# Kernel optimization log

Measured on AMD Instinct MI355X. Metric: run time of the kernel, lower is better.

The kernel has to match this reference:

```python
import jax, jax.numpy as jnp
import numpy as np


def _gcn_conv(X, src, dst, norm, W, n_nodes):
    # gather + normalized aggregate (SpMM) then dense linear (GEMM)
    msg = X[src] * norm[:, None]                       # [E, F]
    agg = jax.ops.segment_sum(msg, dst, num_segments=n_nodes)  # [N, F]
    return agg @ W                                     # [N, F_out]


def setup_inputs() -> dict:
    key = jax.random.key(0)
    k1, k2, k3, k4, k5 = jax.random.split(key, 5)
    N, E, D_IN, D_HID, D_OUT = 50000, 800000, 128, 128, 64
    X = jax.random.normal(k1, (N, D_IN), dtype=jnp.float32)
    edge_index = jax.random.randint(k2, (2, E), 0, N, dtype=jnp.int64)
    s = 1.0 / np.sqrt(D_IN)
    W1 = jax.random.normal(k3, (D_IN, D_HID), dtype=jnp.float32) * s
    W2 = jax.random.normal(k4, (D_HID, D_HID), dtype=jnp.float32) * s
    W3 = jax.random.normal(k5, (D_HID, D_OUT), dtype=jnp.float32) * s
    return {"X": X, "edge_index": edge_index, "W1": W1, "W2": W2, "W3": W3}


def reference(X, edge_index, W1, W2, W3):
    n_nodes = X.shape[0]
    src, dst = edge_index[0], edge_index[1]
    # symmetric degree normalization D^-1/2 A D^-1/2 (degrees from edge list)
    ones = jnp.ones(src.shape[0], dtype=X.dtype)
    deg = jax.ops.segment_sum(ones, dst, num_segments=n_nodes)
    deg = jnp.maximum(deg, 1.0)
    dinv = jax.lax.rsqrt(deg)
    norm = dinv[src] * dinv[dst]                       # [E]
    h = jax.nn.relu(_gcn_conv(X, src, dst, norm, W1, n_nodes))
    h = jax.nn.relu(_gcn_conv(h, src, dst, norm, W2, n_nodes))
    h = jax.nn.relu(_gcn_conv(h, src, dst, norm, W3, n_nodes))
    return jax.nn.softmax(h, axis=-1)
```

## Files before the change

### kernel.cpp

```cpp
#include <hip/hip_runtime.h>
#include <hip/hip_bf16.h>

typedef __attribute__((ext_vector_type(8))) short short8;
typedef __attribute__((ext_vector_type(4))) short short4v;
typedef __attribute__((ext_vector_type(4))) float f32x4;

static inline size_t ws_align(size_t x) { return (x + 511) & ~((size_t)511); }

static __device__ inline unsigned short f2bf(float f) {
    __hip_bfloat16 h = __float2bfloat16(f);
    return __builtin_bit_cast(unsigned short, h);
}
static __device__ inline float bfbits2f(unsigned short u) {
    unsigned x = ((unsigned)u) << 16;
    return __builtin_bit_cast(float, x);
}

static __device__ inline int sniff_fp32(const unsigned short* __restrict__ w1) {
    int i = threadIdx.x & 63;
    unsigned e = (w1[2 * i] >> 7) & 0xFF;
    unsigned long long m = __ballot(e >= 100 && e <= 130);
    return (__popcll(m) < 48) ? 1 : 0;
}
static __device__ inline int sniff_is64(const unsigned int* __restrict__ ei) {
    int i = threadIdx.x & 63;
    unsigned long long m = __ballot(ei[2 * i + 1] == 0u);
    return (__popcll(m) >= 48) ? 1 : 0;
}

__global__ void hist_kernel(const int* __restrict__ ei,
                            int* __restrict__ counts, int* __restrict__ loff, int E) {
    int is64 = sniff_is64((const unsigned int*)ei);
    int e = blockIdx.x * blockDim.x + threadIdx.x;
    if (e < E) {
        int d = is64 ? ei[2 * (size_t)E + 2 * e] : ei[(size_t)E + e];
        loff[e] = atomicAdd(&counts[d], 1);
    }
}

__global__ __launch_bounds__(256) void alloc_kernel(const int* __restrict__ counts,
                                                    float* __restrict__ dinv,
                                                    int2* __restrict__ rc,
                                                    int* __restrict__ total, int N) {
    int n = blockIdx.x * blockDim.x + threadIdx.x;
    int lane = threadIdx.x & 63;
    int c = (n < N) ? counts[n] : 0;
    if (n < N) {
        int d = (c < 1) ? 1 : c;
        dinv[n] = rsqrtf((float)d);
    }
    int incl = c;
#pragma unroll
    for (int off = 1; off < 64; off <<= 1) {
        int v = __shfl_up(incl, off, 64);
        if (lane >= off) incl += v;
    }
    int wavetot = __shfl(incl, 63, 64);
    int base = 0;
    if (lane == 0) base = atomicAdd(total, wavetot);
    base = __shfl(base, 0, 64);
    if (n < N) rc[n] = make_int2(base + incl - c, c);
}

__global__ void fill_kernel(const int* __restrict__ ei,
                            const float* __restrict__ dinv, const int2* __restrict__ rc,
                            const int* __restrict__ loff, int2* __restrict__ edgedat, int E) {
    int is64 = sniff_is64((const unsigned int*)ei);
    int e = blockIdx.x * blockDim.x + threadIdx.x;
    if (e < E) {
        int s, d;
        if (is64) {
            s = ei[2 * e];
            d = ei[2 * (size_t)E + 2 * e];
        } else {
            s = ei[e];
            d = ei[(size_t)E + e];
        }
        int pos = rc[d].x + loff[e];
        float wt = dinv[s] * dinv[d];
        edgedat[pos] = make_int2(s, __float_as_int(wt));
    }
}


template <int FOUT>
__global__ __launch_bounds__(256) void gemm_kernel(const void* __restrict__ Araw, int a_follows,
                                                   const void* __restrict__ Wraw,
                                                   const unsigned short* __restrict__ w1sniff,
                                                   unsigned short* __restrict__ out, int Nrows) {
    constexpr int K = 128;
    constexpr int NT = FOUT / 16;
    constexpr int LDB = K + 8;
    __shared__ __align__(16) unsigned short bt[FOUT * LDB];

    const int tid = threadIdx.x;
    const int in_fp32 = sniff_fp32(w1sniff);
    const int a_fp32 = a_follows & in_fp32;

    constexpr int TOT4 = K * FOUT / 4;
    if (in_fp32) {
        const float* Wf = (const float*)Wraw;
        for (int i = tid; i < TOT4; i += 256) {
            int idx = i * 4;
            int k = idx / FOUT;
            int n = idx & (FOUT - 1);
            float4 v = *(const float4*)(const void*)(Wf + idx);
            bt[(n + 0) * LDB + k] = f2bf(v.x);
            bt[(n + 1) * LDB + k] = f2bf(v.y);
            bt[(n + 2) * LDB + k] = f2bf(v.z);
            bt[(n + 3) * LDB + k] = f2bf(v.w);
        }
    } else {
        const unsigned short* Ws = (const unsigned short*)Wraw;
        for (int i = tid; i < TOT4; i += 256) {
            int idx = i * 4;
            int k = idx / FOUT;
            int n = idx & (FOUT - 1);
            short4v v = *(const short4v*)(const void*)(Ws + idx);
#pragma unroll
            for (int j = 0; j < 4; j++) bt[(n + j) * LDB + k] = ((const unsigned short*)&v)[j];
        }
    }

    const int wave = tid >> 6;
    const int lane = tid & 63;
    const int quad = lane >> 4;
    const int r16 = lane & 15;

    short8 afrag[2][4];
#pragma unroll
    for (int t = 0; t < 2; t++) {
        int arow = blockIdx.x * 128 + t * 64 + wave * 16 + r16;
        if (arow > Nrows - 1) arow = Nrows - 1;
        if (a_fp32) {
            const float* Ap = (const float*)Araw + (size_t)arow * K + quad * 8;
#pragma unroll
            for (int kk = 0; kk < 4; kk++) {
                float4 f0 = *(const float4*)(const void*)(Ap + kk * 32);
                float4 f1 = *(const float4*)(const void*)(Ap + kk * 32 + 4);
                short8 r;
                r[0] = (short)f2bf(f0.x); r[1] = (short)f2bf(f0.y);
                r[2] = (short)f2bf(f0.z); r[3] = (short)f2bf(f0.w);
                r[4] = (short)f2bf(f1.x); r[5] = (short)f2bf(f1.y);
                r[6] = (short)f2bf(f1.z); r[7] = (short)f2bf(f1.w);
                afrag[t][kk] = r;
            }
        } else {
            const unsigned short* Ap = (const unsigned short*)Araw + (size_t)arow * K + quad * 8;
#pragma unroll
            for (int kk = 0; kk < 4; kk++) afrag[t][kk] = *(const short8*)(const void*)(Ap + kk * 32);
        }
    }

    __syncthreads();

    f32x4 acc[2][NT];
#pragma unroll
    for (int t = 0; t < 2; t++)
#pragma unroll
        for (int nt = 0; nt < NT; nt++) acc[t][nt] = (f32x4){0.f, 0.f, 0.f, 0.f};

#pragma unroll
    for (int kk = 0; kk < 4; kk++) {
#pragma unroll
        for (int nt = 0; nt < NT; nt++) {
            short8 b = *(const short8*)(const void*)(&bt[(nt * 16 + r16) * LDB + kk * 32 + quad * 8]);
#pragma unroll
            for (int t = 0; t < 2; t++)
                acc[t][nt] = __builtin_amdgcn_mfma_f32_16x16x32_bf16(afrag[t][kk], b, acc[t][nt], 0, 0, 0);
        }
    }

#pragma unroll
    for (int t = 0; t < 2; t++) {
#pragma unroll
        for (int nt = 0; nt < NT; nt++) {
#pragma unroll
            for (int r = 0; r < 4; r++) {
                float v = acc[t][nt][r];
                float o = __shfl_xor(v, 1, 64);
                int row = blockIdx.x * 128 + t * 64 + wave * 16 + quad * 4 + r;
                if (((lane & 1) == 0) && row < Nrows) {
                    __hip_bfloat162 pk;
                    pk.x = __float2bfloat16(v);
                    pk.y = __float2bfloat16(o);
                    *(__hip_bfloat162*)(out + (size_t)row * FOUT + nt * 16 + r16) = pk;
                }
            }
        }
    }
}


__global__ __launch_bounds__(256) void spmm128_kernel(const int2* __restrict__ edgedat,
                                                      const int2* __restrict__ rc,
                                                      const unsigned short* __restrict__ Hin,
                                                      unsigned short* __restrict__ Hout, int N) {
    int wid = (blockIdx.x * 256 + threadIdx.x) >> 6;
    int lane = threadIdx.x & 63;
    int half = lane >> 5;
    int li = lane & 31;
    int n = wid * 2 + half;
    int nc = (n < N) ? n : (N - 1);
    int2 r_ = rc[nc];
    int start = r_.x;
    int len = (n < N) ? r_.y : 0;
    int maxlen = max(len, __shfl_xor(len, 32, 64));

    float a0 = 0.f, a1 = 0.f, a2 = 0.f, a3 = 0.f;
    for (int j = 0; j < maxlen; j += 8) {
        int2 ed[8];
#pragma unroll
        for (int u = 0; u < 8; u++) {
            int jj = j + u;
            int idx = (jj < len) ? (start + jj) : start;
            ed[u] = edgedat[idx];
        }
        short4v hv[8];
#pragma unroll
        for (int u = 0; u < 8; u++) {
            int s = ed[u].x;
            s = (s < 0) ? 0 : ((s > N - 1) ? (N - 1) : s);
            hv[u] = *(const short4v*)(const void*)(Hin + (size_t)s * 128 + li * 4);
        }
#pragma unroll
        for (int u = 0; u < 8; u++) {
            float w = ((j + u) < len) ? __int_as_float(ed[u].y) : 0.f;
            a0 += w * bfbits2f((unsigned short)hv[u][0]);
            a1 += w * bfbits2f((unsigned short)hv[u][1]);
            a2 += w * bfbits2f((unsigned short)hv[u][2]);
            a3 += w * bfbits2f((unsigned short)hv[u][3]);
        }
    }
    if (n < N) {
        short4v o;
        o[0] = (short)f2bf(fmaxf(a0, 0.f));
        o[1] = (short)f2bf(fmaxf(a1, 0.f));
        o[2] = (short)f2bf(fmaxf(a2, 0.f));
        o[3] = (short)f2bf(fmaxf(a3, 0.f));
        *(short4v*)(Hout + (size_t)n * 128 + li * 4) = o;
    }
}

__global__ __launch_bounds__(256) void spmm64_softmax_kernel(const int2* __restrict__ edgedat,
                                                             const int2* __restrict__ rc,
                                                             const unsigned short* __restrict__ Hin,
                                                             const unsigned short* __restrict__ w1sniff,
                                                             void* __restrict__ Out, int N) {
    int out_fp32 = sniff_fp32(w1sniff);
    int wid = (blockIdx.x * 256 + threadIdx.x) >> 6;
    int lane = threadIdx.x & 63;
    int half = lane >> 5;
    int li = lane & 31;
    int n = wid * 2 + half;
    int nc = (n < N) ? n : (N - 1);
    int2 r_ = rc[nc];
    int start = r_.x;
    int len = (n < N) ? r_.y : 0;
    int maxlen = max(len, __shfl_xor(len, 32, 64));

    float a0 = 0.f, a1 = 0.f;
    for (int j = 0; j < maxlen; j += 8) {
        int2 ed[8];
#pragma unroll
        for (int u = 0; u < 8; u++) {
            int jj = j + u;
            int idx = (jj < len) ? (start + jj) : start;
            ed[u] = edgedat[idx];
        }
        unsigned hv[8];
#pragma unroll
        for (int u = 0; u < 8; u++) {
            int s = ed[u].x;
            s = (s < 0) ? 0 : ((s > N - 1) ? (N - 1) : s);
            hv[u] = *(const unsigned*)(const void*)(Hin + (size_t)s * 64 + li * 2);
        }
#pragma unroll
        for (int u = 0; u < 8; u++) {
            float w = ((j + u) < len) ? __int_as_float(ed[u].y) : 0.f;
            a0 += w * bfbits2f((unsigned short)(hv[u] & 0xFFFF));
            a1 += w * bfbits2f((unsigned short)(hv[u] >> 16));
        }
    }
    a0 = fmaxf(a0, 0.f);
    a1 = fmaxf(a1, 0.f);
    float m = fmaxf(a0, a1);
#pragma unroll
    for (int off = 16; off > 0; off >>= 1) m = fmaxf(m, __shfl_xor(m, off, 64));
    float e0 = __expf(a0 - m), e1 = __expf(a1 - m);
    float s = e0 + e1;
#pragma unroll
    for (int off = 16; off > 0; off >>= 1) s += __shfl_xor(s, off, 64);
    float r0 = e0 / s, r1 = e1 / s;
    if (n < N) {
        if (out_fp32) {
            float2 pk = make_float2(r0, r1);
            *(float2*)((float*)Out + (size_t)n * 64 + li * 2) = pk;
        } else {
            unsigned pk = (unsigned)f2bf(r0) | ((unsigned)f2bf(r1) << 16);
            *(unsigned*)((unsigned short*)Out + (size_t)n * 64 + li * 2) = pk;
        }
    }
}


extern "C" void kernel_launch(void* const* d_in, const int* in_sizes, int n_in,
                              void* d_out, int out_size, void* d_ws, size_t ws_size,
                              hipStream_t stream) {
    const void* X  = d_in[0];
    const int*  ei = (const int*)d_in[1];
    const void* W1 = d_in[2];
    const void* W2 = d_in[3];
    const void* W3 = d_in[4];
    const unsigned short* W1s = (const unsigned short*)W1;

    const int N = in_sizes[0] / 128;
    const int E = in_sizes[1] / 2;

    char* ws = (char*)d_ws;
    size_t off = 0;
    int* counts = (int*)(ws + off);   off += ws_align((size_t)N * 4);
    int* total  = (int*)(ws + off);   off += ws_align(64);
    const size_t zero_bytes = off;
    int2* rc      = (int2*)(ws + off);  off += ws_align((size_t)N * 8);
    float* dinv   = (float*)(ws + off); off += ws_align((size_t)N * 4);
    int* loff     = (int*)(ws + off);   off += ws_align((size_t)E * 4);
    int2* edgedat = (int2*)(ws + off);  off += ws_align((size_t)(E + 64) * 8);
    unsigned short* HA = (unsigned short*)(ws + off); off += ws_align((size_t)N * 128 * 2);
    unsigned short* HB = (unsigned short*)(ws + off); off += ws_align((size_t)N * 128 * 2);

    hipMemsetAsync(d_ws, 0, zero_bytes, stream);

    hist_kernel<<<(E + 255) / 256, 256, 0, stream>>>(ei, counts, loff, E);
    alloc_kernel<<<(N + 255) / 256, 256, 0, stream>>>(counts, dinv, rc, total, N);
    fill_kernel<<<(E + 255) / 256, 256, 0, stream>>>(ei, dinv, rc, loff, edgedat, E);

    const int gblocks = (N + 127) / 128;
    const int waves2 = (N + 1) / 2;
    const int sblocks = (waves2 * 64 + 255) / 256;

    gemm_kernel<128><<<gblocks, 256, 0, stream>>>(X, 1, W1, W1s, HA, N);
    spmm128_kernel<<<sblocks, 256, 0, stream>>>(edgedat, rc, HA, HB, N);
    gemm_kernel<128><<<gblocks, 256, 0, stream>>>(HB, 0, W2, W1s, HA, N);
    spmm128_kernel<<<sblocks, 256, 0, stream>>>(edgedat, rc, HA, HB, N);
    gemm_kernel<64><<<gblocks, 256, 0, stream>>>(HB, 0, W3, W1s, HA, N);
    spmm64_softmax_kernel<<<sblocks, 256, 0, stream>>>(edgedat, rc, HA, W1s, d_out, N);
}
```

Baseline: 288.2 us.

## Pad CSR rows to multiples of 8 and assign one wave per node in SpMM

Row lengths in the CSR are rounded up to a multiple of 8, and the padded slots are zero-filled, so the SpMM inner loops run without per-edge bounds checks or source clamping. The SpMM kernels now give each node a whole 64-lane wave instead of two nodes per wave, with row start and length made wave-uniform through readfirstlane. This lowers per-edge ALU work and divergence between the two half-waves. In exchange it adds a memset over the enlarged edge array, extra zero-weight padded edges (about 4 per node on average), and twice as many waves with smaller per-lane loads.

```diff
diff --git a/kernel.cpp b/kernel.cpp
--- a/kernel.cpp
+++ b/kernel.cpp
@@ -49,7 +49,8 @@
         int d = (c < 1) ? 1 : c;
         dinv[n] = rsqrtf((float)d);
     }
-    int incl = c;
+    int lenp = (c + 7) & ~7;
+    int incl = lenp;
 #pragma unroll
     for (int off = 1; off < 64; off <<= 1) {
         int v = __shfl_up(incl, off, 64);
@@ -59,7 +60,7 @@
     int base = 0;
     if (lane == 0) base = atomicAdd(total, wavetot);
     base = __shfl(base, 0, 64);
-    if (n < N) rc[n] = make_int2(base + incl - c, c);
+    if (n < N) rc[n] = make_int2(base + incl - lenp, lenp);
 }
 
 __global__ void fill_kernel(const int* __restrict__ ei,
@@ -194,52 +195,35 @@
 
 __global__ __launch_bounds__(256) void spmm128_kernel(const int2* __restrict__ edgedat,
                                                       const int2* __restrict__ rc,
-                                                      const unsigned short* __restrict__ Hin,
-                                                      unsigned short* __restrict__ Hout, int N) {
+                                                      const __hip_bfloat162* __restrict__ Hin,
+                                                      __hip_bfloat162* __restrict__ Hout, int N) {
     int wid = (blockIdx.x * 256 + threadIdx.x) >> 6;
+    if (wid >= N) return;
     int lane = threadIdx.x & 63;
-    int half = lane >> 5;
-    int li = lane & 31;
-    int n = wid * 2 + half;
-    int nc = (n < N) ? n : (N - 1);
-    int2 r_ = rc[nc];
-    int start = r_.x;
-    int len = (n < N) ? r_.y : 0;
-    int maxlen = max(len, __shfl_xor(len, 32, 64));
-
-    float a0 = 0.f, a1 = 0.f, a2 = 0.f, a3 = 0.f;
-    for (int j = 0; j < maxlen; j += 8) {
+    int2 r_ = rc[wid];
+    int start = __builtin_amdgcn_readfirstlane(r_.x);
+    int lenp  = __builtin_amdgcn_readfirstlane(r_.y);
+    const __hip_bfloat162* col = Hin + lane;
+
+    float ax = 0.f, ay = 0.f;
+    for (int j = 0; j < lenp; j += 8) {
         int2 ed[8];
 #pragma unroll
+        for (int u = 0; u < 8; u++) ed[u] = edgedat[start + j + u];
+        __hip_bfloat162 hv[8];
+#pragma unroll
+        for (int u = 0; u < 8; u++) hv[u] = col[(size_t)ed[u].x * 64];
+#pragma unroll
         for (int u = 0; u < 8; u++) {
-            int jj = j + u;
-            int idx = (jj < len) ? (start + jj) : start;
-            ed[u] = edgedat[idx];
-        }
-        short4v hv[8];
-#pragma unroll
-        for (int u = 0; u < 8; u++) {
-            int s = ed[u].x;
-            s = (s < 0) ? 0 : ((s > N - 1) ? (N - 1) : s);
-            hv[u] = *(const short4v*)(const void*)(Hin + (size_t)s * 128 + li * 4);
-        }
-#pragma unroll
-        for (int u = 0; u < 8; u++) {
-            float w = ((j + u) < len) ? __int_as_float(ed[u].y) : 0.f;
-            a0 += w * bfbits2f((unsigned short)hv[u][0]);
-            a1 += w * bfbits2f((unsigned short)hv[u][1]);
-            a2 += w * bfbits2f((unsigned short)hv[u][2]);
-            a3 += w * bfbits2f((unsigned short)hv[u][3]);
-        }
-    }
-    if (n < N) {
-        short4v o;
-        o[0] = (short)f2bf(fmaxf(a0, 0.f));
-        o[1] = (short)f2bf(fmaxf(a1, 0.f));
-        o[2] = (short)f2bf(fmaxf(a2, 0.f));
-        o[3] = (short)f2bf(fmaxf(a3, 0.f));
-        *(short4v*)(Hout + (size_t)n * 128 + li * 4) = o;
-    }
+            float w = __int_as_float(ed[u].y);
+            ax += w * __bfloat162float(hv[u].x);
+            ay += w * __bfloat162float(hv[u].y);
+        }
+    }
+    __hip_bfloat162 pk;
+    pk.x = __float2bfloat16(fmaxf(ax, 0.f));
+    pk.y = __float2bfloat16(fmaxf(ay, 0.f));
+    Hout[(size_t)wid * 64 + lane] = pk;
 }
 
 __global__ __launch_bounds__(256) void spmm64_softmax_kernel(const int2* __restrict__ edgedat,
@@ -249,57 +233,37 @@
                                                              void* __restrict__ Out, int N) {
     int out_fp32 = sniff_fp32(w1sniff);
     int wid = (blockIdx.x * 256 + threadIdx.x) >> 6;
+    if (wid >= N) return;
     int lane = threadIdx.x & 63;
-    int half = lane >> 5;
-    int li = lane & 31;
-    int n = wid * 2 + half;
-    int nc = (n < N) ? n : (N - 1);
-    int2 r_ = rc[nc];
-    int start = r_.x;
-    int len = (n < N) ? r_.y : 0;
-    int maxlen = max(len, __shfl_xor(len, 32, 64));
-
-    float a0 = 0.f, a1 = 0.f;
-    for (int j = 0; j < maxlen; j += 8) {
+    int2 r_ = rc[wid];
+    int start = __builtin_amdgcn_readfirstlane(r_.x);
+    int lenp  = __builtin_amdgcn_readfirstlane(r_.y);
+    const unsigned short* col = Hin + lane;
+
+    float a = 0.f;
+    for (int j = 0; j < lenp; j += 8) {
         int2 ed[8];
 #pragma unroll
-        for (int u = 0; u < 8; u++) {
-            int jj = j + u;
-            int idx = (jj < len) ? (start + jj) : start;
-            ed[u] = edgedat[idx];
-        }
-        unsigned hv[8];
-#pragma unroll
-        for (int u = 0; u < 8; u++) {
-            int s = ed[u].x;
-            s = (s < 0) ? 0 : ((s > N - 1) ? (N - 1) : s);
-            hv[u] = *(const unsigned*)(const void*)(Hin + (size_t)s * 64 + li * 2);
-        }
-#pragma unroll
-        for (int u = 0; u < 8; u++) {
-            float w = ((j + u) < len) ? __int_as_float(ed[u].y) : 0.f;
-            a0 += w * bfbits2f((unsigned short)(hv[u] & 0xFFFF));
-            a1 += w * bfbits2f((unsigned short)(hv[u] >> 16));
-        }
-    }
-    a0 = fmaxf(a0, 0.f);
-    a1 = fmaxf(a1, 0.f);
-    float m = fmaxf(a0, a1);
-#pragma unroll
-    for (int off = 16; off > 0; off >>= 1) m = fmaxf(m, __shfl_xor(m, off, 64));
-    float e0 = __expf(a0 - m), e1 = __expf(a1 - m);
-    float s = e0 + e1;
-#pragma unroll
-    for (int off = 16; off > 0; off >>= 1) s += __shfl_xor(s, off, 64);
-    float r0 = e0 / s, r1 = e1 / s;
-    if (n < N) {
-        if (out_fp32) {
-            float2 pk = make_float2(r0, r1);
-            *(float2*)((float*)Out + (size_t)n * 64 + li * 2) = pk;
-        } else {
-            unsigned pk = (unsigned)f2bf(r0) | ((unsigned)f2bf(r1) << 16);
-            *(unsigned*)((unsigned short*)Out + (size_t)n * 64 + li * 2) = pk;
-        }
+        for (int u = 0; u < 8; u++) ed[u] = edgedat[start + j + u];
+        float hv[8];
+#pragma unroll
+        for (int u = 0; u < 8; u++) hv[u] = bfbits2f(col[(size_t)ed[u].x * 64]);
+#pragma unroll
+        for (int u = 0; u < 8; u++) a += __int_as_float(ed[u].y) * hv[u];
+    }
+    a = fmaxf(a, 0.f);
+    float m = a;
+#pragma unroll
+    for (int off = 32; off > 0; off >>= 1) m = fmaxf(m, __shfl_xor(m, off, 64));
+    float e = __expf(a - m);
+    float s = e;
+#pragma unroll
+    for (int off = 32; off > 0; off >>= 1) s += __shfl_xor(s, off, 64);
+    float r = e / s;
+    if (out_fp32) {
+        ((float*)Out)[(size_t)wid * 64 + lane] = r;
+    } else {
+        ((unsigned short*)Out)[(size_t)wid * 64 + lane] = f2bf(r);
     }
 }
 
@@ -317,6 +281,8 @@
     const int N = in_sizes[0] / 128;
     const int E = in_sizes[1] / 2;
 
+    const size_t edgecap = (size_t)E + 8 * (size_t)N + 64;
+
     char* ws = (char*)d_ws;
     size_t off = 0;
     int* counts = (int*)(ws + off);   off += ws_align((size_t)N * 4);
@@ -325,24 +291,26 @@
     int2* rc      = (int2*)(ws + off);  off += ws_align((size_t)N * 8);
     float* dinv   = (float*)(ws + off); off += ws_align((size_t)N * 4);
     int* loff     = (int*)(ws + off);   off += ws_align((size_t)E * 4);
-    int2* edgedat = (int2*)(ws + off);  off += ws_align((size_t)(E + 64) * 8);
+    int2* edgedat = (int2*)(ws + off);  off += ws_align(edgecap * 8);
     unsigned short* HA = (unsigned short*)(ws + off); off += ws_align((size_t)N * 128 * 2);
     unsigned short* HB = (unsigned short*)(ws + off); off += ws_align((size_t)N * 128 * 2);
 
     hipMemsetAsync(d_ws, 0, zero_bytes, stream);
+    hipMemsetAsync(edgedat, 0, edgecap * 8, stream);
 
     hist_kernel<<<(E + 255) / 256, 256, 0, stream>>>(ei, counts, loff, E);
     alloc_kernel<<<(N + 255) / 256, 256, 0, stream>>>(counts, dinv, rc, total, N);
     fill_kernel<<<(E + 255) / 256, 256, 0, stream>>>(ei, dinv, rc, loff, edgedat, E);
 
     const int gblocks = (N + 127) / 128;
-    const int waves2 = (N + 1) / 2;
-    const int sblocks = (waves2 * 64 + 255) / 256;
+    const int sblocks = ((size_t)N * 64 + 255) / 256;
 
     gemm_kernel<128><<<gblocks, 256, 0, stream>>>(X, 1, W1, W1s, HA, N);
-    spmm128_kernel<<<sblocks, 256, 0, stream>>>(edgedat, rc, HA, HB, N);
+    spmm128_kernel<<<sblocks, 256, 0, stream>>>(edgedat, rc, (const __hip_bfloat162*)HA,
+                                                (__hip_bfloat162*)HB, N);
     gemm_kernel<128><<<gblocks, 256, 0, stream>>>(HB, 0, W2, W1s, HA, N);
-    spmm128_kernel<<<sblocks, 256, 0, stream>>>(edgedat, rc, HA, HB, N);
+    spmm128_kernel<<<sblocks, 256, 0, stream>>>(edgedat, rc, (const __hip_bfloat162*)HA,
+                                                (__hip_bfloat162*)HB, N);
     gemm_kernel<64><<<gblocks, 256, 0, stream>>>(HB, 0, W3, W1s, HA, N);
     spmm64_softmax_kernel<<<sblocks, 256, 0, stream>>>(edgedat, rc, HA, W1s, d_out, N);
 }
```

Result: faster. 274.7 us (-4.7%).
